# Kernel tuning notes

Measured on AMD Instinct MI355X. Metric: run time of the kernel, lower is better.

## Reference

```python
import jax, jax.numpy as jnp
import numpy as np

K = 20  # n_knn

def knn_idx(x, k):
    # x: (B, C, N) -> (B, N, k) indices of k nearest neighbors (by neg sq dist)
    xx = jnp.sum(x * x, axis=1)                      # (B, N)
    inner = jnp.einsum('bcn,bcm->bnm', x, x)          # (B, N, N)
    neg_dist = 2.0 * inner - xx[:, :, None] - xx[:, None, :]
    _, idx = jax.lax.top_k(neg_dist, k)               # (B, N, k)
    return idx

def get_graph_feature(x, k):
    # x: (B, C, N) -> (B, 2C, N, k) with channels [x_j - x_i, x_i]
    idx = knn_idx(x, k)                               # (B, N, k)
    feats = jnp.transpose(x, (0, 2, 1))               # (B, N, C)
    neighbors = jax.vmap(lambda f, i: f[i])(feats, idx)   # (B, N, k, C)
    center = feats[:, :, None, :]                     # (B, N, 1, C)
    center_b = jnp.broadcast_to(center, neighbors.shape)
    feat = jnp.concatenate([neighbors - center_b, center_b], axis=-1)  # (B,N,k,2C)
    return jnp.transpose(feat, (0, 3, 1, 2))          # (B, 2C, N, k)

def edge_conv(x, w, s, b, k):
    # 1x1 conv (no bias) + folded eval-BN affine + LeakyReLU(0.2), then max over k
    g = get_graph_feature(x, k)                       # (B, 2C, N, k)
    y = jnp.einsum('bcnk,oc->bonk', g, w)
    y = y * s[None, :, None, None] + b[None, :, None, None]
    y = jnp.where(y >= 0, y, 0.2 * y)
    return jnp.max(y, axis=-1)                        # (B, O, N)

def setup_inputs() -> dict:
    key = jax.random.key(0)
    ks = jax.random.split(key, 16)
    d = {'x': jax.random.normal(ks[0], (16, 3, 1024), dtype=jnp.float32)}
    dims = [(64, 6), (64, 128), (128, 128), (256, 256), (512, 512)]
    for i, (o, c) in enumerate(dims):
        d[f'w{i+1}'] = jax.random.normal(ks[3*i+1], (o, c), dtype=jnp.float32) * (1.0 / np.sqrt(c))
        d[f's{i+1}'] = jax.random.uniform(ks[3*i+2], (o,), dtype=jnp.float32, minval=0.5, maxval=1.5)
        d[f'b{i+1}'] = jax.random.normal(ks[3*i+3], (o,), dtype=jnp.float32) * 0.1
    return d

def reference(x, w1, s1, b1, w2, s2, b2, w3, s3, b3, w4, s4, b4, w5, s5, b5):
    x1 = edge_conv(x, w1, s1, b1, K)    # (B, 64, N)
    x2 = edge_conv(x1, w2, s2, b2, K)   # (B, 64, N)
    x3 = edge_conv(x2, w3, s3, b3, K)   # (B, 128, N)
    x4 = edge_conv(x3, w4, s4, b4, K)   # (B, 256, N)
    xc = jnp.concatenate([x1, x2, x3, x4], axis=1)  # (B, 512, N)
    y = jnp.einsum('bcn,oc->bon', xc, w5)
    y = y * s5[None, :, None] + b5[None, :, None]
    x_inv = jnp.where(y >= 0, y, 0.2 * y)            # (B, feat_dim, N)
    p_max = jnp.max(x_inv, axis=-1)                  # (B, feat_dim)
    p_avg = jnp.mean(x_inv, axis=-1)                 # (B, feat_dim)
    x_equ = jnp.concatenate([p_max, p_avg], axis=1)  # (B, 2*feat_dim)
    return (x_equ, x_inv)
```

## Files before the change

### kernel.cpp

```cpp
#include <hip/hip_runtime.h>
#include <hip/hip_bf16.h>

#define NPTS 1024
#define KNN_K 20

template<int C>
__global__ __launch_bounds__(256)
void knn_kernel(const float* __restrict__ x, int* __restrict__ knn_idx,
                int in_bstride)
{
    __shared__ float dist[8][NPTS];
    __shared__ float xn[8][C];
    __shared__ float xxr[8];
    const int b  = blockIdx.x >> 7;
    const int n0 = (blockIdx.x & 127) << 3;
    const int tid = threadIdx.x;
    const float* xb = x + (size_t)b * in_bstride;

    for (int i = tid; i < 8 * C; i += 256) {
        const int r = i / C, c = i - r * C;
        xn[r][c] = xb[c * NPTS + n0 + r];
    }
    __syncthreads();
    if (tid < 8) {
        float s = 0.f;
        for (int c = 0; c < C; c++) s = fmaf(xn[tid][c], xn[tid][c], s);
        xxr[tid] = s;
    }
    __syncthreads();

    float acc[8][4];
    #pragma unroll
    for (int r = 0; r < 8; r++)
        acc[r][0] = acc[r][1] = acc[r][2] = acc[r][3] = 0.f;
    float sq[4] = {0.f, 0.f, 0.f, 0.f};
    const int m0 = tid * 4;
    #pragma unroll 4
    for (int c = 0; c < C; c++) {
        const float4 xm = *reinterpret_cast<const float4*>(xb + c * NPTS + m0);
        sq[0] = fmaf(xm.x, xm.x, sq[0]);
        sq[1] = fmaf(xm.y, xm.y, sq[1]);
        sq[2] = fmaf(xm.z, xm.z, sq[2]);
        sq[3] = fmaf(xm.w, xm.w, sq[3]);
        #pragma unroll
        for (int r = 0; r < 8; r++) {
            const float xv = xn[r][c];
            acc[r][0] = fmaf(xv, xm.x, acc[r][0]);
            acc[r][1] = fmaf(xv, xm.y, acc[r][1]);
            acc[r][2] = fmaf(xv, xm.z, acc[r][2]);
            acc[r][3] = fmaf(xv, xm.w, acc[r][3]);
        }
    }
    #pragma unroll
    for (int r = 0; r < 8; r++) {
        float4 dv;
        dv.x = 2.f * acc[r][0] - xxr[r] - sq[0];
        dv.y = 2.f * acc[r][1] - xxr[r] - sq[1];
        dv.z = 2.f * acc[r][2] - xxr[r] - sq[2];
        dv.w = 2.f * acc[r][3] - xxr[r] - sq[3];
        *reinterpret_cast<float4*>(&dist[r][m0]) = dv;
    }
    __syncthreads();

    const int r    = tid >> 5;
    const int lane = tid & 31;
    float v[32];
    #pragma unroll
    for (int q = 0; q < 32; q++) v[q] = dist[r][lane + 32 * q];

    float lv = v[0]; int lq = 0;
    #pragma unroll
    for (int q = 1; q < 32; q++) if (v[q] > lv) { lv = v[q]; lq = q; }

    int* outp = knn_idx + ((size_t)(b * NPTS + n0 + r)) * KNN_K;
    for (int k = 0; k < KNN_K; k++) {
        float bv_ = lv;
        int   bm  = lane + 32 * lq;
        #pragma unroll
        for (int off = 16; off; off >>= 1) {
            const float ov = __shfl_xor(bv_, off, 32);
            const int   om = __shfl_xor(bm, off, 32);
            if (ov > bv_ || (ov == bv_ && om < bm)) { bv_ = ov; bm = om; }
        }
        if (lane == 0) outp[k] = bm;
        const int wl = bm & 31, wq = bm >> 5;
        if (lane == wl) {
            #pragma unroll
            for (int q = 0; q < 32; q++) if (q == wq) v[q] = -INFINITY;
            lv = v[0]; lq = 0;
            #pragma unroll
            for (int q = 1; q < 32; q++) if (v[q] > lv) { lv = v[q]; lq = q; }
        }
    }
}

template<bool DUAL>
__global__ __launch_bounds__(256)
void mm_kernel(const float* __restrict__ xin, const float* __restrict__ w,
               float* __restrict__ Z, float* __restrict__ Z2,
               int C, int O, int in_bstride, int wstride)
{
    __shared__ float xs[32][64];
    __shared__ float ws1[32][68];
    __shared__ float ws2[32][68];
    const int n0 = blockIdx.x * 64;
    const int o0 = blockIdx.y * 64;
    const int b  = blockIdx.z;
    const int tid = threadIdx.x;
    const int nl = (tid & 15) * 4;
    const int ol = (tid >> 4) * 4;
    float a1[4][4] = {{0.f}};
    float a2[4][4] = {{0.f}};
    const float* xb = xin + (size_t)b * in_bstride;

    for (int cc = 0; cc < C; cc += 32) {
        #pragma unroll
        for (int t = 0; t < 8; t++) {
            const int id = tid + t * 256;
            const int j = id >> 6, nn = id & 63;
            const int c = cc + j;
            xs[j][nn] = (c < C) ? xb[c * NPTS + n0 + nn] : 0.f;
        }
        #pragma unroll
        for (int t = 0; t < 8; t++) {
            const int id = tid + t * 256;
            const int j = id & 31, i = id >> 5;
            const int c = cc + j;
            ws1[j][i] = (c < C) ? w[(o0 + i) * wstride + c] : 0.f;
            if (DUAL) ws2[j][i] = (c < C) ? w[(o0 + i) * wstride + C + c] : 0.f;
        }
        __syncthreads();
        #pragma unroll
        for (int j = 0; j < 32; j++) {
            const float4 xv = *reinterpret_cast<const float4*>(&xs[j][nl]);
            const float4 wv = *reinterpret_cast<const float4*>(&ws1[j][ol]);
            const float xr[4] = {xv.x, xv.y, xv.z, xv.w};
            const float wr[4] = {wv.x, wv.y, wv.z, wv.w};
            #pragma unroll
            for (int oi = 0; oi < 4; oi++)
                #pragma unroll
                for (int ni = 0; ni < 4; ni++)
                    a1[oi][ni] = fmaf(wr[oi], xr[ni], a1[oi][ni]);
            if (DUAL) {
                const float4 w2 = *reinterpret_cast<const float4*>(&ws2[j][ol]);
                const float w2r[4] = {w2.x, w2.y, w2.z, w2.w};
                #pragma unroll
                for (int oi = 0; oi < 4; oi++)
                    #pragma unroll
                    for (int ni = 0; ni < 4; ni++)
                        a2[oi][ni] = fmaf(w2r[oi], xr[ni], a2[oi][ni]);
            }
        }
        __syncthreads();
    }

    #pragma unroll
    for (int oi = 0; oi < 4; oi++) {
        const int o = o0 + ol + oi;
        const float4 r1 = make_float4(a1[oi][0], a1[oi][1], a1[oi][2], a1[oi][3]);
        *reinterpret_cast<float4*>(Z + ((size_t)b * O + o) * NPTS + n0 + nl) = r1;
        if (DUAL) {
            const float4 r2 = make_float4(a2[oi][0], a2[oi][1], a2[oi][2], a2[oi][3]);
            *reinterpret_cast<float4*>(Z2 + ((size_t)b * O + o) * NPTS + n0 + nl) = r2;
        }
    }
}

__global__ __launch_bounds__(256)
void mm5_kernel(const float* __restrict__ xin, const float* __restrict__ w,
                const float* __restrict__ sv, const float* __restrict__ bvec,
                float* __restrict__ out)
{
    __shared__ float xs[32][128];
    __shared__ float ws[32][128];
    const int n0 = blockIdx.x * 128;
    const int o0 = blockIdx.y * 128;
    const int b  = blockIdx.z;
    const int tid = threadIdx.x;
    const int nl = (tid & 15) * 8;
    const int ol = (tid >> 4) * 8;
    float acc[8][8] = {{0.f}};
    const float* xb = xin + (size_t)b * (512 * NPTS);

    for (int cc = 0; cc < 512; cc += 32) {
        #pragma unroll
        for (int t = 0; t < 4; t++) {
            const int f = tid + t * 256;
            const int j = f >> 5, col = (f & 31) * 4;
            *reinterpret_cast<float4*>(&xs[j][col]) =
                *reinterpret_cast<const float4*>(&xb[(cc + j) * NPTS + n0 + col]);
        }
        #pragma unroll
        for (int t = 0; t < 4; t++) {
            const int id = tid + t * 256;
            const int i = id & 127, jq = (id >> 7) * 4;
            const float4 wv = *reinterpret_cast<const float4*>(&w[(o0 + i) * 512 + cc + jq]);
            ws[jq + 0][i] = wv.x;
            ws[jq + 1][i] = wv.y;
            ws[jq + 2][i] = wv.z;
            ws[jq + 3][i] = wv.w;
        }
        __syncthreads();
        #pragma unroll
        for (int j = 0; j < 32; j++) {
            float xr[8], wr[8];
            *reinterpret_cast<float4*>(&xr[0]) = *reinterpret_cast<const float4*>(&xs[j][nl]);
            *reinterpret_cast<float4*>(&xr[4]) = *reinterpret_cast<const float4*>(&xs[j][nl + 4]);
            *reinterpret_cast<float4*>(&wr[0]) = *reinterpret_cast<const float4*>(&ws[j][ol]);
            *reinterpret_cast<float4*>(&wr[4]) = *reinterpret_cast<const float4*>(&ws[j][ol + 4]);
            #pragma unroll
            for (int oi = 0; oi < 8; oi++)
                #pragma unroll
                for (int ni = 0; ni < 8; ni++)
                    acc[oi][ni] = fmaf(wr[oi], xr[ni], acc[oi][ni]);
        }
        __syncthreads();
    }

    #pragma unroll
    for (int oi = 0; oi < 8; oi++) {
        const int o = o0 + ol + oi;
        const float s = sv[o], bb = bvec[o];
        float* zp = out + ((size_t)b * 512 + o) * NPTS + n0 + nl;
        #pragma unroll
        for (int h = 0; h < 2; h++) {
            float4 r;
            r.x = fmaf(s, acc[oi][h * 4 + 0], bb);
            r.y = fmaf(s, acc[oi][h * 4 + 1], bb);
            r.z = fmaf(s, acc[oi][h * 4 + 2], bb);
            r.w = fmaf(s, acc[oi][h * 4 + 3], bb);
            r.x = r.x >= 0.f ? r.x : 0.2f * r.x;
            r.y = r.y >= 0.f ? r.y : 0.2f * r.y;
            r.z = r.z >= 0.f ? r.z : 0.2f * r.z;
            r.w = r.w >= 0.f ? r.w : 0.2f * r.w;
            *reinterpret_cast<float4*>(zp + h * 4) = r;
        }
    }
}

__global__ __launch_bounds__(256)
void gather_kernel(const float* __restrict__ Z, const float* __restrict__ Z2,
                   const int* __restrict__ knn_idx,
                   const float* __restrict__ sv, const float* __restrict__ bvec,
                   float* __restrict__ outc, int O, int ch_off)
{
    __shared__ int idx_s[64][21];
    const int n0  = blockIdx.x * 64;
    const int og0 = blockIdx.y * 16;
    const int b   = blockIdx.z;
    const int tid = threadIdx.x;
    const int* ig = knn_idx + (size_t)(b * NPTS + n0) * KNN_K;
    for (int i = tid; i < 64 * KNN_K; i += 256) {
        const int nn = i / KNN_K, k = i - nn * KNN_K;
        idx_s[nn][k] = ig[i];
    }
    __syncthreads();
    const int nn = tid & 63;
    const int oo = tid >> 6;
    const int n  = n0 + nn;
    for (int oc = 0; oc < 16; oc += 4) {
        const int o = og0 + oc + oo;
        const float* zr = Z + ((size_t)b * O + o) * NPTS;
        float mx = -INFINITY;
        #pragma unroll
        for (int k = 0; k < KNN_K; k++)
            mx = fmaxf(mx, zr[idx_s[nn][k]]);
        const float cz = zr[n];
        const float z2 = Z2[((size_t)b * O + o) * NPTS + n];
        float y = fmaf(sv[o], (mx - cz + z2), bvec[o]);
        y = y >= 0.f ? y : 0.2f * y;
        outc[(size_t)b * (512 * NPTS) + (size_t)(ch_off + o) * NPTS + n] = y;
    }
}

__global__ __launch_bounds__(256)
void reduce_kernel(const float* __restrict__ xinv, float* __restrict__ xequ)
{
    const int b = blockIdx.x >> 9;
    const int o = blockIdx.x & 511;
    const float* row = xinv + (size_t)blockIdx.x * NPTS;
    const int tid = threadIdx.x;
    const float4 val = *reinterpret_cast<const float4*>(&row[tid * 4]);
    float mx = fmaxf(fmaxf(val.x, val.y), fmaxf(val.z, val.w));
    float sm = (val.x + val.y) + (val.z + val.w);
    #pragma unroll
    for (int off = 32; off; off >>= 1) {
        mx = fmaxf(mx, __shfl_down(mx, off));
        sm += __shfl_down(sm, off);
    }
    __shared__ float smx[4], ssm[4];
    if ((tid & 63) == 0) { smx[tid >> 6] = mx; ssm[tid >> 6] = sm; }
    __syncthreads();
    if (tid == 0) {
        mx = fmaxf(fmaxf(smx[0], smx[1]), fmaxf(smx[2], smx[3]));
        sm = (ssm[0] + ssm[1]) + (ssm[2] + ssm[3]);
        xequ[b * 1024 + o] = mx;
        xequ[b * 1024 + 512 + o] = sm * (1.0f / 1024.0f);
    }
}

extern "C" void kernel_launch(void* const* d_in, const int* in_sizes, int n_in,
                              void* d_out, int out_size, void* d_ws, size_t ws_size,
                              hipStream_t stream)
{
    const float* x  = (const float*)d_in[0];
    const float* w1 = (const float*)d_in[1],  *s1 = (const float*)d_in[2],  *b1 = (const float*)d_in[3];
    const float* w2 = (const float*)d_in[4],  *s2 = (const float*)d_in[5],  *b2 = (const float*)d_in[6];
    const float* w3 = (const float*)d_in[7],  *s3 = (const float*)d_in[8],  *b3 = (const float*)d_in[9];
    const float* w4 = (const float*)d_in[10], *s4 = (const float*)d_in[11], *b4 = (const float*)d_in[12];
    const float* w5 = (const float*)d_in[13], *s5 = (const float*)d_in[14], *b5 = (const float*)d_in[15];

    float* out  = (float*)d_out;
    float* xequ = out;
    float* xinv = out + 16 * 1024;

    float* xc  = (float*)d_ws;
    float* Z   = xc  + (size_t)16 * 512 * NPTS;
    float* Z2  = Z   + (size_t)16 * 256 * NPTS;
    int*   idxb = (int*)(Z2 + (size_t)16 * 256 * NPTS);

    const int BS_XC = 512 * NPTS;

    knn_kernel<3><<<2048, 256, 0, stream>>>(x, idxb, 3 * NPTS);
    mm_kernel<true><<<dim3(16, 1, 16), 256, 0, stream>>>(
        x, w1, Z, Z2, 3, 64, 3 * NPTS, 6);
    gather_kernel<<<dim3(16, 4, 16), 256, 0, stream>>>(Z, Z2, idxb, s1, b1, xc, 64, 0);

    knn_kernel<64><<<2048, 256, 0, stream>>>(xc, idxb, BS_XC);
    mm_kernel<true><<<dim3(16, 1, 16), 256, 0, stream>>>(
        xc, w2, Z, Z2, 64, 64, BS_XC, 128);
    gather_kernel<<<dim3(16, 4, 16), 256, 0, stream>>>(Z, Z2, idxb, s2, b2, xc, 64, 64);

    {
        const float* in3 = xc + (size_t)64 * NPTS;
        knn_kernel<64><<<2048, 256, 0, stream>>>(in3, idxb, BS_XC);
        mm_kernel<true><<<dim3(16, 2, 16), 256, 0, stream>>>(
            in3, w3, Z, Z2, 64, 128, BS_XC, 128);
        gather_kernel<<<dim3(16, 8, 16), 256, 0, stream>>>(Z, Z2, idxb, s3, b3, xc, 128, 128);
    }

    {
        const float* in4 = xc + (size_t)128 * NPTS;
        knn_kernel<128><<<2048, 256, 0, stream>>>(in4, idxb, BS_XC);
        mm_kernel<true><<<dim3(16, 4, 16), 256, 0, stream>>>(
            in4, w4, Z, Z2, 128, 256, BS_XC, 256);
        gather_kernel<<<dim3(16, 16, 16), 256, 0, stream>>>(Z, Z2, idxb, s4, b4, xc, 256, 256);
    }

    mm5_kernel<<<dim3(8, 4, 16), 256, 0, stream>>>(xc, w5, s5, b5, xinv);

    reduce_kernel<<<8192, 256, 0, stream>>>(xinv, xequ);
}
```

Before: 831.1 us.

## Widen KNN blocks to 512 threads with 64-lane top-k and shrink mm5 tile

The KNN kernel now uses 512 threads per block. Each thread computes 2 distance columns instead of 4, and the centre-point features are read from shared memory as float4 when C is a multiple of 4. Top-k selection now uses a full 64-lane wavefront per query row with 16 register values per lane, instead of 32 lanes with 32 values, which cuts register pressure and the serial scan length but adds one more shuffle stage. The final mm5 GEMM tile drops from 128x128 to 64 outputs x 128 points, doubling the grid for more occupancy at the cost of reloading the activation tile more often.

```diff
diff --git a/kernel.cpp b/kernel.cpp
--- a/kernel.cpp
+++ b/kernel.cpp
@@ -5,7 +5,7 @@
 #define KNN_K 20
 
 template<int C>
-__global__ __launch_bounds__(256)
+__global__ __launch_bounds__(512, 6)
 void knn_kernel(const float* __restrict__ x, int* __restrict__ knn_idx,
                 int in_bstride)
 {
@@ -17,7 +17,7 @@
     const int tid = threadIdx.x;
     const float* xb = x + (size_t)b * in_bstride;
 
-    for (int i = tid; i < 8 * C; i += 256) {
+    for (int i = tid; i < 8 * C; i += 512) {
         const int r = i / C, c = i - r * C;
         xn[r][c] = xb[c * NPTS + n0 + r];
     }
@@ -29,67 +29,82 @@
     }
     __syncthreads();
 
-    float acc[8][4];
-    #pragma unroll
-    for (int r = 0; r < 8; r++)
-        acc[r][0] = acc[r][1] = acc[r][2] = acc[r][3] = 0.f;
-    float sq[4] = {0.f, 0.f, 0.f, 0.f};
-    const int m0 = tid * 4;
-    #pragma unroll 4
-    for (int c = 0; c < C; c++) {
-        const float4 xm = *reinterpret_cast<const float4*>(xb + c * NPTS + m0);
-        sq[0] = fmaf(xm.x, xm.x, sq[0]);
-        sq[1] = fmaf(xm.y, xm.y, sq[1]);
-        sq[2] = fmaf(xm.z, xm.z, sq[2]);
-        sq[3] = fmaf(xm.w, xm.w, sq[3]);
-        #pragma unroll
-        for (int r = 0; r < 8; r++) {
-            const float xv = xn[r][c];
-            acc[r][0] = fmaf(xv, xm.x, acc[r][0]);
-            acc[r][1] = fmaf(xv, xm.y, acc[r][1]);
-            acc[r][2] = fmaf(xv, xm.z, acc[r][2]);
-            acc[r][3] = fmaf(xv, xm.w, acc[r][3]);
+    float acc[8][2];
+    #pragma unroll
+    for (int r = 0; r < 8; r++) acc[r][0] = acc[r][1] = 0.f;
+    float sq[2] = {0.f, 0.f};
+    const int m0 = tid * 2;
+
+    if constexpr (C % 4 == 0) {
+        for (int c4 = 0; c4 < C; c4 += 4) {
+            float4 xnv[8];
+            #pragma unroll
+            for (int r = 0; r < 8; r++)
+                xnv[r] = *reinterpret_cast<const float4*>(&xn[r][c4]);
+            #pragma unroll
+            for (int u = 0; u < 4; u++) {
+                const float2 xm = *reinterpret_cast<const float2*>(xb + (c4 + u) * NPTS + m0);
+                sq[0] = fmaf(xm.x, xm.x, sq[0]);
+                sq[1] = fmaf(xm.y, xm.y, sq[1]);
+                #pragma unroll
+                for (int r = 0; r < 8; r++) {
+                    const float xv = (u == 0) ? xnv[r].x : (u == 1) ? xnv[r].y
+                                   : (u == 2) ? xnv[r].z : xnv[r].w;
+                    acc[r][0] = fmaf(xv, xm.x, acc[r][0]);
+                    acc[r][1] = fmaf(xv, xm.y, acc[r][1]);
+                }
+            }
+        }
+    } else {
+        for (int c = 0; c < C; c++) {
+            const float2 xm = *reinterpret_cast<const float2*>(xb + c * NPTS + m0);
+            sq[0] = fmaf(xm.x, xm.x, sq[0]);
+            sq[1] = fmaf(xm.y, xm.y, sq[1]);
+            #pragma unroll
+            for (int r = 0; r < 8; r++) {
+                const float xv = xn[r][c];
+                acc[r][0] = fmaf(xv, xm.x, acc[r][0]);
+                acc[r][1] = fmaf(xv, xm.y, acc[r][1]);
+            }
         }
     }
     #pragma unroll
     for (int r = 0; r < 8; r++) {
-        float4 dv;
+        float2 dv;
         dv.x = 2.f * acc[r][0] - xxr[r] - sq[0];
         dv.y = 2.f * acc[r][1] - xxr[r] - sq[1];
-        dv.z = 2.f * acc[r][2] - xxr[r] - sq[2];
-        dv.w = 2.f * acc[r][3] - xxr[r] - sq[3];
-        *reinterpret_cast<float4*>(&dist[r][m0]) = dv;
-    }
-    __syncthreads();
-
-    const int r    = tid >> 5;
-    const int lane = tid & 31;
-    float v[32];
-    #pragma unroll
-    for (int q = 0; q < 32; q++) v[q] = dist[r][lane + 32 * q];
+        *reinterpret_cast<float2*>(&dist[r][m0]) = dv;
+    }
+    __syncthreads();
+
+    const int r    = tid >> 6;
+    const int lane = tid & 63;
+    float v[16];
+    #pragma unroll
+    for (int q = 0; q < 16; q++) v[q] = dist[r][lane + 64 * q];
 
     float lv = v[0]; int lq = 0;
     #pragma unroll
-    for (int q = 1; q < 32; q++) if (v[q] > lv) { lv = v[q]; lq = q; }
+    for (int q = 1; q < 16; q++) if (v[q] > lv) { lv = v[q]; lq = q; }
 
     int* outp = knn_idx + ((size_t)(b * NPTS + n0 + r)) * KNN_K;
     for (int k = 0; k < KNN_K; k++) {
         float bv_ = lv;
-        int   bm  = lane + 32 * lq;
-        #pragma unroll
-        for (int off = 16; off; off >>= 1) {
-            const float ov = __shfl_xor(bv_, off, 32);
-            const int   om = __shfl_xor(bm, off, 32);
+        int   bm  = lane + 64 * lq;
+        #pragma unroll
+        for (int off = 32; off; off >>= 1) {
+            const float ov = __shfl_xor(bv_, off);
+            const int   om = __shfl_xor(bm, off);
             if (ov > bv_ || (ov == bv_ && om < bm)) { bv_ = ov; bm = om; }
         }
         if (lane == 0) outp[k] = bm;
-        const int wl = bm & 31, wq = bm >> 5;
+        const int wl = bm & 63, wq = bm >> 6;
         if (lane == wl) {
             #pragma unroll
-            for (int q = 0; q < 32; q++) if (q == wq) v[q] = -INFINITY;
+            for (int q = 0; q < 16; q++) if (q == wq) v[q] = -INFINITY;
             lv = v[0]; lq = 0;
             #pragma unroll
-            for (int q = 1; q < 32; q++) if (v[q] > lv) { lv = v[q]; lq = q; }
+            for (int q = 1; q < 16; q++) if (v[q] > lv) { lv = v[q]; lq = q; }
         }
     }
 }
@@ -166,20 +181,20 @@
     }
 }
 
-__global__ __launch_bounds__(256)
+__global__ __launch_bounds__(256, 4)
 void mm5_kernel(const float* __restrict__ xin, const float* __restrict__ w,
                 const float* __restrict__ sv, const float* __restrict__ bvec,
                 float* __restrict__ out)
 {
     __shared__ float xs[32][128];
-    __shared__ float ws[32][128];
+    __shared__ float ws[32][68];
     const int n0 = blockIdx.x * 128;
-    const int o0 = blockIdx.y * 128;
+    const int o0 = blockIdx.y * 64;
     const int b  = blockIdx.z;
     const int tid = threadIdx.x;
     const int nl = (tid & 15) * 8;
-    const int ol = (tid >> 4) * 8;
-    float acc[8][8] = {{0.f}};
+    const int ol = (tid >> 4) * 4;
+    float acc[4][8] = {{0.f}};
     const float* xb = xin + (size_t)b * (512 * NPTS);
 
     for (int cc = 0; cc < 512; cc += 32) {
@@ -191,9 +206,9 @@
                 *reinterpret_cast<const float4*>(&xb[(cc + j) * NPTS + n0 + col]);
         }
         #pragma unroll
-        for (int t = 0; t < 4; t++) {
+        for (int t = 0; t < 2; t++) {
             const int id = tid + t * 256;
-            const int i = id & 127, jq = (id >> 7) * 4;
+            const int i = id & 63, jq = (id >> 6) * 4;
             const float4 wv = *reinterpret_cast<const float4*>(&w[(o0 + i) * 512 + cc + jq]);
             ws[jq + 0][i] = wv.x;
             ws[jq + 1][i] = wv.y;
@@ -203,13 +218,12 @@
         __syncthreads();
         #pragma unroll
         for (int j = 0; j < 32; j++) {
-            float xr[8], wr[8];
+            float xr[8], wr[4];
             *reinterpret_cast<float4*>(&xr[0]) = *reinterpret_cast<const float4*>(&xs[j][nl]);
             *reinterpret_cast<float4*>(&xr[4]) = *reinterpret_cast<const float4*>(&xs[j][nl + 4]);
             *reinterpret_cast<float4*>(&wr[0]) = *reinterpret_cast<const float4*>(&ws[j][ol]);
-            *reinterpret_cast<float4*>(&wr[4]) = *reinterpret_cast<const float4*>(&ws[j][ol + 4]);
-            #pragma unroll
-            for (int oi = 0; oi < 8; oi++)
+            #pragma unroll
+            for (int oi = 0; oi < 4; oi++)
                 #pragma unroll
                 for (int ni = 0; ni < 8; ni++)
                     acc[oi][ni] = fmaf(wr[oi], xr[ni], acc[oi][ni]);
@@ -218,7 +232,7 @@
     }
 
     #pragma unroll
-    for (int oi = 0; oi < 8; oi++) {
+    for (int oi = 0; oi < 4; oi++) {
         const int o = o0 + ol + oi;
         const float s = sv[o], bb = bvec[o];
         float* zp = out + ((size_t)b * 512 + o) * NPTS + n0 + nl;
@@ -321,19 +335,19 @@
 
     const int BS_XC = 512 * NPTS;
 
-    knn_kernel<3><<<2048, 256, 0, stream>>>(x, idxb, 3 * NPTS);
+    knn_kernel<3><<<2048, 512, 0, stream>>>(x, idxb, 3 * NPTS);
     mm_kernel<true><<<dim3(16, 1, 16), 256, 0, stream>>>(
         x, w1, Z, Z2, 3, 64, 3 * NPTS, 6);
     gather_kernel<<<dim3(16, 4, 16), 256, 0, stream>>>(Z, Z2, idxb, s1, b1, xc, 64, 0);
 
-    knn_kernel<64><<<2048, 256, 0, stream>>>(xc, idxb, BS_XC);
+    knn_kernel<64><<<2048, 512, 0, stream>>>(xc, idxb, BS_XC);
     mm_kernel<true><<<dim3(16, 1, 16), 256, 0, stream>>>(
         xc, w2, Z, Z2, 64, 64, BS_XC, 128);
     gather_kernel<<<dim3(16, 4, 16), 256, 0, stream>>>(Z, Z2, idxb, s2, b2, xc, 64, 64);
 
     {
         const float* in3 = xc + (size_t)64 * NPTS;
-        knn_kernel<64><<<2048, 256, 0, stream>>>(in3, idxb, BS_XC);
+        knn_kernel<64><<<2048, 512, 0, stream>>>(in3, idxb, BS_XC);
         mm_kernel<true><<<dim3(16, 2, 16), 256, 0, stream>>>(
             in3, w3, Z, Z2, 64, 128, BS_XC, 128);
         gather_kernel<<<dim3(16, 8, 16), 256, 0, stream>>>(Z, Z2, idxb, s3, b3, xc, 128, 128);
@@ -341,13 +355,13 @@
 
     {
         const float* in4 = xc + (size_t)128 * NPTS;
-        knn_kernel<128><<<2048, 256, 0, stream>>>(in4, idxb, BS_XC);
+        knn_kernel<128><<<2048, 512, 0, stream>>>(in4, idxb, BS_XC);
         mm_kernel<true><<<dim3(16, 4, 16), 256, 0, stream>>>(
             in4, w4, Z, Z2, 128, 256, BS_XC, 256);
         gather_kernel<<<dim3(16, 16, 16), 256, 0, stream>>>(Z, Z2, idxb, s4, b4, xc, 256, 256);
     }
 
-    mm5_kernel<<<dim3(8, 4, 16), 256, 0, stream>>>(xc, w5, s5, b5, xinv);
+    mm5_kernel<<<dim3(8, 8, 16), 256, 0, stream>>>(xc, w5, s5, b5, xinv);
 
     reduce_kernel<<<8192, 256, 0, stream>>>(xinv, xequ);
 }
```

Result: slower. 953.3 us (+14.7%).
